# Kernel tuning notes

Hardware: AMD Instinct MI355X
Metric: run time of the kernel (lower is better)

Reference implementation:

```python
import jax, jax.numpy as jnp
import numpy as np

E, T, D_IN, D_INT = 8, 512, 7168, 2048


def setup_inputs() -> dict:
    key = jax.random.key(0)
    ks = jax.random.split(key, 7)
    return {
        "x": jax.random.normal(ks[0], (E, T, D_IN), dtype=jnp.float32),
        "w1": jax.random.normal(ks[1], (E, D_INT, D_IN), dtype=jnp.float32),
        "b1": jax.random.normal(ks[2], (E, D_INT), dtype=jnp.float32),
        "w3": jax.random.normal(ks[3], (E, D_INT, D_IN), dtype=jnp.float32),
        "b3": jax.random.normal(ks[4], (E, D_INT), dtype=jnp.float32),
        "w2": jax.random.normal(ks[5], (E, D_IN, D_INT), dtype=jnp.float32),
        "b2": jax.random.normal(ks[6], (E, D_IN), dtype=jnp.float32),
    }


def reference(x, w1, b1, w3, b3, w2, b2):
    # Batched (per-expert) SwiGLU FFN: w2(silu(w1(x)) * w3(x)), all with bias.
    # e: expert, t: token, d: in_channels, f: inter_channels
    h1 = jnp.einsum("etd,efd->etf", x, w1) + b1[:, None, :]  # [E,T,F]
    h3 = jnp.einsum("etd,efd->etf", x, w3) + b3[:, None, :]  # [E,T,F]
    g = jax.nn.silu(h1) * h3                                  # [E,T,F]
    return jnp.einsum("etf,edf->etd", g, w2) + b2[:, None, :]  # [E,T,D]
```

## Files before the change

kernel.cpp:

```cpp
#include <hip/hip_runtime.h>
#include <hip/hip_bf16.h>

#define NE 8
#define NT 512
#define DIN 7168
#define DINT 2048
#define BK 64

typedef __bf16 bf16x8 __attribute__((ext_vector_type(8)));
typedef float f32x4 __attribute__((ext_vector_type(4)));
typedef unsigned short ushort8v __attribute__((ext_vector_type(8)));

#define MFMA __builtin_amdgcn_mfma_f32_16x16x32_bf16

__device__ __forceinline__ int swz(int row, int k) {
    return (row << 6) + (((k >> 3) ^ (row & 7)) << 3) + (k & 7);
}

__device__ __forceinline__ ushort4 cvt4(float4 v) {
    ushort4 h;
    h.x = __builtin_bit_cast(unsigned short, (__bf16)v.x);
    h.y = __builtin_bit_cast(unsigned short, (__bf16)v.y);
    h.z = __builtin_bit_cast(unsigned short, (__bf16)v.z);
    h.w = __builtin_bit_cast(unsigned short, (__bf16)v.w);
    return h;
}

__device__ __forceinline__ void barrier_lgkm() {
    asm volatile("s_waitcnt lgkmcnt(0)" ::: "memory");
    __builtin_amdgcn_s_barrier();
}

__global__ __launch_bounds__(512, 2) void ffn_gate_up(
    const float* __restrict__ x, const float* __restrict__ w1,
    const float* __restrict__ b1, const float* __restrict__ w3,
    const float* __restrict__ b3, unsigned short* __restrict__ g) {
    __shared__ unsigned short As[2][256 * BK];
    __shared__ unsigned short B1s[2][128 * BK];
    __shared__ unsigned short B3s[2][128 * BK];

    const int tid = threadIdx.x;
    const int lane = tid & 63;
    const int wave = tid >> 6;
    const int wm = wave >> 1, wn = wave & 1;
    const int e = blockIdx.z;
    const int bn = blockIdx.x * 128;
    const int bm = blockIdx.y * 256;

    const char* xb = (const char*)x + ((size_t)e * NT * DIN + (size_t)bm * DIN) * 4;
    const char* w1c = (const char*)w1 + ((size_t)e * DINT * DIN + (size_t)bn * DIN) * 4;
    const char* w3c = (const char*)w3 + ((size_t)e * DINT * DIN + (size_t)bn * DIN) * 4;

    const int srow = tid >> 4;
    const int scol = (tid & 15) * 4;
    const int swb = swz(srow, scol);

    int xo[8];
#pragma unroll
    for (int p = 0; p < 8; ++p) xo[p] = ((p * 32 + srow) * DIN + scol) * 4;

    f32x4 acc1[4][4], acc3[4][4];
#pragma unroll
    for (int m = 0; m < 4; ++m)
#pragma unroll
        for (int n = 0; n < 4; ++n) {
            acc1[m][n] = (f32x4)0.0f;
            acc3[m][n] = (f32x4)0.0f;
        }

    float4 ra[8], rb1[4], rb3[4];

#pragma unroll
    for (int p = 0; p < 8; ++p) ra[p] = *(const float4*)(xb + xo[p]);
#pragma unroll
    for (int p = 0; p < 4; ++p) {
        rb1[p] = *(const float4*)(w1c + xo[p]);
        rb3[p] = *(const float4*)(w3c + xo[p]);
    }
#pragma unroll
    for (int p = 0; p < 8; ++p) *(ushort4*)&As[0][p * 2048 + swb] = cvt4(ra[p]);
#pragma unroll
    for (int p = 0; p < 4; ++p) {
        *(ushort4*)&B1s[0][p * 2048 + swb] = cvt4(rb1[p]);
        *(ushort4*)&B3s[0][p * 2048 + swb] = cvt4(rb3[p]);
    }
#pragma unroll
    for (int p = 0; p < 8; ++p) ra[p] = *(const float4*)(xb + xo[p] + BK * 4);
#pragma unroll
    for (int p = 0; p < 4; ++p) {
        rb1[p] = *(const float4*)(w1c + xo[p] + BK * 4);
        rb3[p] = *(const float4*)(w3c + xo[p] + BK * 4);
    }
    barrier_lgkm();

    const int l15 = lane & 15;
    const int kf0 = (lane >> 4) << 3;

    int cur = 0;
    const int NIT = DIN / BK;
    for (int t = 0; t < NIT; ++t) {
        const int nxt = cur ^ 1;
        const int kldB = ((t + 2 < NIT) ? (t + 2) * BK : (NIT - 1) * BK) * 4;
        const bool stage = (t < NIT - 1);
        bf16x8 af[4], bb[4];

#pragma unroll
        for (int m = 0; m < 4; ++m)
            af[m] = *(const bf16x8*)&As[cur][swz(wm * 64 + m * 16 + l15, kf0)];
#pragma unroll
        for (int n = 0; n < 4; ++n)
            bb[n] = *(const bf16x8*)&B1s[cur][swz(wn * 64 + n * 16 + l15, kf0)];
        if (stage) {
#pragma unroll
            for (int p = 0; p < 4; ++p) *(ushort4*)&As[nxt][p * 2048 + swb] = cvt4(ra[p]);
#pragma unroll
            for (int p = 0; p < 4; ++p) ra[p] = *(const float4*)(xb + xo[p] + kldB);
        }
        __builtin_amdgcn_s_setprio(1);
#pragma unroll
        for (int n = 0; n < 4; ++n)
#pragma unroll
            for (int m = 0; m < 4; ++m)
                acc1[m][n] = MFMA(af[m], bb[n], acc1[m][n], 0, 0, 0);
        __builtin_amdgcn_s_setprio(0);
        __builtin_amdgcn_sched_barrier(0);

#pragma unroll
        for (int n = 0; n < 4; ++n)
            bb[n] = *(const bf16x8*)&B3s[cur][swz(wn * 64 + n * 16 + l15, kf0)];
        if (stage) {
#pragma unroll
            for (int p = 4; p < 8; ++p) *(ushort4*)&As[nxt][p * 2048 + swb] = cvt4(ra[p]);
#pragma unroll
            for (int p = 4; p < 8; ++p) ra[p] = *(const float4*)(xb + xo[p] + kldB);
        }
        __builtin_amdgcn_s_setprio(1);
#pragma unroll
        for (int n = 0; n < 4; ++n)
#pragma unroll
            for (int m = 0; m < 4; ++m)
                acc3[m][n] = MFMA(af[m], bb[n], acc3[m][n], 0, 0, 0);
        __builtin_amdgcn_s_setprio(0);
        __builtin_amdgcn_sched_barrier(0);

#pragma unroll
        for (int m = 0; m < 4; ++m)
            af[m] = *(const bf16x8*)&As[cur][swz(wm * 64 + m * 16 + l15, 32 + kf0)];
#pragma unroll
        for (int n = 0; n < 4; ++n)
            bb[n] = *(const bf16x8*)&B1s[cur][swz(wn * 64 + n * 16 + l15, 32 + kf0)];
        if (stage) {
#pragma unroll
            for (int p = 0; p < 4; ++p) *(ushort4*)&B1s[nxt][p * 2048 + swb] = cvt4(rb1[p]);
#pragma unroll
            for (int p = 0; p < 4; ++p) rb1[p] = *(const float4*)(w1c + xo[p] + kldB);
        }
        __builtin_amdgcn_s_setprio(1);
#pragma unroll
        for (int n = 0; n < 4; ++n)
#pragma unroll
            for (int m = 0; m < 4; ++m)
                acc1[m][n] = MFMA(af[m], bb[n], acc1[m][n], 0, 0, 0);
        __builtin_amdgcn_s_setprio(0);
        __builtin_amdgcn_sched_barrier(0);

#pragma unroll
        for (int n = 0; n < 4; ++n)
            bb[n] = *(const bf16x8*)&B3s[cur][swz(wn * 64 + n * 16 + l15, 32 + kf0)];
        if (stage) {
#pragma unroll
            for (int p = 0; p < 4; ++p) *(ushort4*)&B3s[nxt][p * 2048 + swb] = cvt4(rb3[p]);
#pragma unroll
            for (int p = 0; p < 4; ++p) rb3[p] = *(const float4*)(w3c + xo[p] + kldB);
        }
        __builtin_amdgcn_s_setprio(1);
#pragma unroll
        for (int n = 0; n < 4; ++n)
#pragma unroll
            for (int m = 0; m < 4; ++m)
                acc3[m][n] = MFMA(af[m], bb[n], acc3[m][n], 0, 0, 0);
        __builtin_amdgcn_s_setprio(0);

        barrier_lgkm();
        cur = nxt;
    }

    float bias1[4], bias3[4];
#pragma unroll
    for (int n = 0; n < 4; ++n) {
        const int f = bn + wn * 64 + n * 16 + l15;
        bias1[n] = b1[e * DINT + f];
        bias3[n] = b3[e * DINT + f];
    }
#pragma unroll
    for (int m = 0; m < 4; ++m)
#pragma unroll
        for (int n = 0; n < 4; ++n) {
            const int f = bn + wn * 64 + n * 16 + l15;
#pragma unroll
            for (int j = 0; j < 4; ++j) {
                const int t = bm + wm * 64 + m * 16 + ((lane >> 4) << 2) + j;
                const float h1 = acc1[m][n][j] + bias1[n];
                const float h3 = acc3[m][n][j] + bias3[n];
                const float sg = h1 / (1.0f + __expf(-h1));
                g[(size_t)e * NT * DINT + (size_t)t * DINT + f] =
                    __builtin_bit_cast(unsigned short, (__bf16)(sg * h3));
            }
        }
}

__global__ __launch_bounds__(512, 2) void ffn_down(
    const unsigned short* __restrict__ g, const float* __restrict__ w2,
    const float* __restrict__ b2, float* __restrict__ out) {
    __shared__ unsigned short As[2][256 * BK];
    __shared__ unsigned short Bs[2][128 * BK];

    const int tid = threadIdx.x;
    const int lane = tid & 63;
    const int wave = tid >> 6;
    const int wm = wave >> 1, wn = wave & 1;
    const int e = blockIdx.z;
    const int bn = blockIdx.x * 128;
    const int bm = blockIdx.y * 256;

    const char* gc = (const char*)g + ((size_t)e * NT * DINT + (size_t)bm * DINT) * 2;
    const char* w2c = (const char*)w2 + ((size_t)e * DIN * DINT + (size_t)bn * DINT) * 4;

    const int arow = tid >> 3;
    const int acol = (tid & 7) * 8;
    const int brow = tid >> 4;
    const int bcol = (tid & 15) * 4;
    const int swA = swz(arow, acol);
    const int swB = swz(brow, bcol);

    int go[4], wo[4];
#pragma unroll
    for (int p = 0; p < 4; ++p) {
        go[p] = ((p * 64 + arow) * DINT + acol) * 2;
        wo[p] = ((p * 32 + brow) * DINT + bcol) * 4;
    }

    f32x4 acc[4][4];
#pragma unroll
    for (int m = 0; m < 4; ++m)
#pragma unroll
        for (int n = 0; n < 4; ++n) acc[m][n] = (f32x4)0.0f;

    ushort8v ga[4];
    float4 rb[4];

#pragma unroll
    for (int p = 0; p < 4; ++p) ga[p] = *(const ushort8v*)(gc + go[p]);
#pragma unroll
    for (int p = 0; p < 4; ++p) rb[p] = *(const float4*)(w2c + wo[p]);
#pragma unroll
    for (int p = 0; p < 4; ++p) *(ushort8v*)&As[0][p * 4096 + swA] = ga[p];
#pragma unroll
    for (int p = 0; p < 4; ++p) *(ushort4*)&Bs[0][p * 2048 + swB] = cvt4(rb[p]);
#pragma unroll
    for (int p = 0; p < 4; ++p) ga[p] = *(const ushort8v*)(gc + go[p] + BK * 2);
#pragma unroll
    for (int p = 0; p < 4; ++p) rb[p] = *(const float4*)(w2c + wo[p] + BK * 4);
    barrier_lgkm();

    const int l15 = lane & 15;
    const int kf0 = (lane >> 4) << 3;

    int cur = 0;
    const int NIT = DINT / BK;
    for (int t = 0; t < NIT; ++t) {
        const int nxt = cur ^ 1;
        const int kld = (t + 2 < NIT) ? (t + 2) * BK : (NIT - 1) * BK;
        const bool stage = (t < NIT - 1);
        bf16x8 af[4], bf[4];

#pragma unroll
        for (int m = 0; m < 4; ++m)
            af[m] = *(const bf16x8*)&As[cur][swz(wm * 64 + m * 16 + l15, kf0)];
#pragma unroll
        for (int n = 0; n < 4; ++n)
            bf[n] = *(const bf16x8*)&Bs[cur][swz(wn * 64 + n * 16 + l15, kf0)];
        if (stage) {
#pragma unroll
            for (int p = 0; p < 4; ++p) *(ushort8v*)&As[nxt][p * 4096 + swA] = ga[p];
#pragma unroll
            for (int p = 0; p < 4; ++p) ga[p] = *(const ushort8v*)(gc + go[p] + kld * 2);
        }
        __builtin_amdgcn_s_setprio(1);
#pragma unroll
        for (int n = 0; n < 4; ++n)
#pragma unroll
            for (int m = 0; m < 4; ++m)
                acc[m][n] = MFMA(af[m], bf[n], acc[m][n], 0, 0, 0);
        __builtin_amdgcn_s_setprio(0);
        __builtin_amdgcn_sched_barrier(0);

#pragma unroll
        for (int m = 0; m < 4; ++m)
            af[m] = *(const bf16x8*)&As[cur][swz(wm * 64 + m * 16 + l15, 32 + kf0)];
#pragma unroll
        for (int n = 0; n < 4; ++n)
            bf[n] = *(const bf16x8*)&Bs[cur][swz(wn * 64 + n * 16 + l15, 32 + kf0)];
        if (stage) {
#pragma unroll
            for (int p = 0; p < 4; ++p) *(ushort4*)&Bs[nxt][p * 2048 + swB] = cvt4(rb[p]);
#pragma unroll
            for (int p = 0; p < 4; ++p) rb[p] = *(const float4*)(w2c + wo[p] + kld * 4);
        }
        __builtin_amdgcn_s_setprio(1);
#pragma unroll
        for (int n = 0; n < 4; ++n)
#pragma unroll
            for (int m = 0; m < 4; ++m)
                acc[m][n] = MFMA(af[m], bf[n], acc[m][n], 0, 0, 0);
        __builtin_amdgcn_s_setprio(0);

        barrier_lgkm();
        cur = nxt;
    }

    float bias[4];
#pragma unroll
    for (int n = 0; n < 4; ++n) {
        const int d = bn + wn * 64 + n * 16 + l15;
        bias[n] = b2[e * DIN + d];
    }
#pragma unroll
    for (int m = 0; m < 4; ++m)
#pragma unroll
        for (int n = 0; n < 4; ++n) {
            const int d = bn + wn * 64 + n * 16 + l15;
#pragma unroll
            for (int j = 0; j < 4; ++j) {
                const int t = bm + wm * 64 + m * 16 + ((lane >> 4) << 2) + j;
                out[(size_t)e * NT * DIN + (size_t)t * DIN + d] = acc[m][n][j] + bias[n];
            }
        }
}

extern "C" void kernel_launch(void* const* d_in, const int* in_sizes, int n_in,
                              void* d_out, int out_size, void* d_ws, size_t ws_size,
                              hipStream_t stream) {
    const float* x = (const float*)d_in[0];
    const float* w1 = (const float*)d_in[1];
    const float* b1 = (const float*)d_in[2];
    const float* w3 = (const float*)d_in[3];
    const float* b3 = (const float*)d_in[4];
    const float* w2 = (const float*)d_in[5];
    const float* b2 = (const float*)d_in[6];
    float* out = (float*)d_out;
    unsigned short* g = (unsigned short*)d_ws;

    dim3 gridA(DINT / 128, NT / 256, NE);
    dim3 gridB(DIN / 128, NT / 256, NE);
    ffn_gate_up<<<gridA, dim3(512), 0, stream>>>(x, w1, b1, w3, b3, g);
    ffn_down<<<gridB, dim3(512), 0, stream>>>(g, w2, b2, out);
}
```

Measured before the change: 502.0 us.

## Use 8-wide LDS stores and per-phase barriers for ping-pong wave scheduling

Staging now has each thread load two adjacent float4s, 32 contiguous bytes per row, and write them to LDS as one 16-byte bf16x8 store instead of two 8-byte stores. This halves the LDS store instruction count. The single end-of-iteration barrier is replaced by s_barrier calls around every MFMA phase, so waves alternate between memory and compute in lockstep, a ping-pong schedule. Global loads now run unconditionally, clamped to the last tile. The extra barriers add sync overhead per iteration and may stall waves if the phases are unbalanced.

Measured after the change: 523.9 us. 4.4% more time.

```diff
diff --git a/kernel.cpp b/kernel.cpp
--- a/kernel.cpp
+++ b/kernel.cpp
@@ -17,19 +17,20 @@
     return (row << 6) + (((k >> 3) ^ (row & 7)) << 3) + (k & 7);
 }
 
-__device__ __forceinline__ ushort4 cvt4(float4 v) {
-    ushort4 h;
-    h.x = __builtin_bit_cast(unsigned short, (__bf16)v.x);
-    h.y = __builtin_bit_cast(unsigned short, (__bf16)v.y);
-    h.z = __builtin_bit_cast(unsigned short, (__bf16)v.z);
-    h.w = __builtin_bit_cast(unsigned short, (__bf16)v.w);
+__device__ __forceinline__ unsigned short b16(float f) {
+    return __builtin_bit_cast(unsigned short, (__bf16)f);
+}
+__device__ __forceinline__ ushort8v cvt8(float4 a, float4 b) {
+    ushort8v h;
+    h[0] = b16(a.x); h[1] = b16(a.y); h[2] = b16(a.z); h[3] = b16(a.w);
+    h[4] = b16(b.x); h[5] = b16(b.y); h[6] = b16(b.z); h[7] = b16(b.w);
     return h;
 }
 
-__device__ __forceinline__ void barrier_lgkm() {
-    asm volatile("s_waitcnt lgkmcnt(0)" ::: "memory");
-    __builtin_amdgcn_s_barrier();
-}
+#define PHASE_BAR()                                        \
+    __builtin_amdgcn_s_barrier();                          \
+    asm volatile("s_waitcnt lgkmcnt(0)" ::: "memory");     \
+    __builtin_amdgcn_sched_barrier(0)
 
 __global__ __launch_bounds__(512, 2) void ffn_gate_up(
     const float* __restrict__ x, const float* __restrict__ w1,
@@ -51,13 +52,16 @@
     const char* w1c = (const char*)w1 + ((size_t)e * DINT * DIN + (size_t)bn * DIN) * 4;
     const char* w3c = (const char*)w3 + ((size_t)e * DINT * DIN + (size_t)bn * DIN) * 4;
 
-    const int srow = tid >> 4;
-    const int scol = (tid & 15) * 4;
-    const int swb = swz(srow, scol);
-
-    int xo[8];
-#pragma unroll
-    for (int p = 0; p < 8; ++p) xo[p] = ((p * 32 + srow) * DIN + scol) * 4;
+    const int srow = tid >> 3;
+    const int sc8 = (tid & 7) * 8;
+    const int scB = (tid & 7) * 32;
+    const int swb = swz(srow, sc8);
+
+    int xoA[4], xoB[2];
+#pragma unroll
+    for (int p = 0; p < 4; ++p) xoA[p] = (p * 64 + srow) * DIN * 4 + scB;
+#pragma unroll
+    for (int p = 0; p < 2; ++p) xoB[p] = (p * 64 + srow) * DIN * 4 + scB;
 
     f32x4 acc1[4][4], acc3[4][4];
 #pragma unroll
@@ -71,27 +75,39 @@
     float4 ra[8], rb1[4], rb3[4];
 
 #pragma unroll
-    for (int p = 0; p < 8; ++p) ra[p] = *(const float4*)(xb + xo[p]);
-#pragma unroll
     for (int p = 0; p < 4; ++p) {
-        rb1[p] = *(const float4*)(w1c + xo[p]);
-        rb3[p] = *(const float4*)(w3c + xo[p]);
-    }
-#pragma unroll
-    for (int p = 0; p < 8; ++p) *(ushort4*)&As[0][p * 2048 + swb] = cvt4(ra[p]);
+        ra[2 * p] = *(const float4*)(xb + xoA[p]);
+        ra[2 * p + 1] = *(const float4*)(xb + xoA[p] + 16);
+    }
+#pragma unroll
+    for (int p = 0; p < 2; ++p) {
+        rb1[2 * p] = *(const float4*)(w1c + xoB[p]);
+        rb1[2 * p + 1] = *(const float4*)(w1c + xoB[p] + 16);
+        rb3[2 * p] = *(const float4*)(w3c + xoB[p]);
+        rb3[2 * p + 1] = *(const float4*)(w3c + xoB[p] + 16);
+    }
+#pragma unroll
+    for (int p = 0; p < 4; ++p)
+        *(ushort8v*)&As[0][p * 4096 + swb] = cvt8(ra[2 * p], ra[2 * p + 1]);
+#pragma unroll
+    for (int p = 0; p < 2; ++p) {
+        *(ushort8v*)&B1s[0][p * 4096 + swb] = cvt8(rb1[2 * p], rb1[2 * p + 1]);
+        *(ushort8v*)&B3s[0][p * 4096 + swb] = cvt8(rb3[2 * p], rb3[2 * p + 1]);
+    }
 #pragma unroll
     for (int p = 0; p < 4; ++p) {
-        *(ushort4*)&B1s[0][p * 2048 + swb] = cvt4(rb1[p]);
-        *(ushort4*)&B3s[0][p * 2048 + swb] = cvt4(rb3[p]);
-    }
-#pragma unroll
-    for (int p = 0; p < 8; ++p) ra[p] = *(const float4*)(xb + xo[p] + BK * 4);
-#pragma unroll
-    for (int p = 0; p < 4; ++p) {
-        rb1[p] = *(const float4*)(w1c + xo[p] + BK * 4);
-        rb3[p] = *(const float4*)(w3c + xo[p] + BK * 4);
-    }
-    barrier_lgkm();
+        ra[2 * p] = *(const float4*)(xb + xoA[p] + BK * 4);
+        ra[2 * p + 1] = *(const float4*)(xb + xoA[p] + BK * 4 + 16);
+    }
+#pragma unroll
+    for (int p = 0; p < 2; ++p) {
+        rb1[2 * p] = *(const float4*)(w1c + xoB[p] + BK * 4);
+        rb1[2 * p + 1] = *(const float4*)(w1c + xoB[p] + BK * 4 + 16);
+        rb3[2 * p] = *(const float4*)(w3c + xoB[p] + BK * 4);
+        rb3[2 * p + 1] = *(const float4*)(w3c + xoB[p] + BK * 4 + 16);
+    }
+    asm volatile("s_waitcnt lgkmcnt(0)" ::: "memory");
+    __builtin_amdgcn_s_barrier();
 
     const int l15 = lane & 15;
     const int kf0 = (lane >> 4) << 3;
@@ -100,7 +116,7 @@
     const int NIT = DIN / BK;
     for (int t = 0; t < NIT; ++t) {
         const int nxt = cur ^ 1;
-        const int kldB = ((t + 2 < NIT) ? (t + 2) * BK : (NIT - 1) * BK) * 4;
+        const int kldB = ((t + 2 < NIT) ? (t + 2) : (NIT - 1)) * BK * 4;
         const bool stage = (t < NIT - 1);
         bf16x8 af[4], bb[4];
 
@@ -111,11 +127,14 @@
         for (int n = 0; n < 4; ++n)
             bb[n] = *(const bf16x8*)&B1s[cur][swz(wn * 64 + n * 16 + l15, kf0)];
         if (stage) {
-#pragma unroll
-            for (int p = 0; p < 4; ++p) *(ushort4*)&As[nxt][p * 2048 + swb] = cvt4(ra[p]);
-#pragma unroll
-            for (int p = 0; p < 4; ++p) ra[p] = *(const float4*)(xb + xo[p] + kldB);
-        }
+            *(ushort8v*)&As[nxt][0 * 4096 + swb] = cvt8(ra[0], ra[1]);
+            *(ushort8v*)&As[nxt][1 * 4096 + swb] = cvt8(ra[2], ra[3]);
+        }
+        ra[0] = *(const float4*)(xb + xoA[0] + kldB);
+        ra[1] = *(const float4*)(xb + xoA[0] + kldB + 16);
+        ra[2] = *(const float4*)(xb + xoA[1] + kldB);
+        ra[3] = *(const float4*)(xb + xoA[1] + kldB + 16);
+        PHASE_BAR();
         __builtin_amdgcn_s_setprio(1);
 #pragma unroll
         for (int n = 0; n < 4; ++n)
@@ -123,17 +142,20 @@
             for (int m = 0; m < 4; ++m)
                 acc1[m][n] = MFMA(af[m], bb[n], acc1[m][n], 0, 0, 0);
         __builtin_amdgcn_s_setprio(0);
-        __builtin_amdgcn_sched_barrier(0);
+        __builtin_amdgcn_s_barrier();
 
 #pragma unroll
         for (int n = 0; n < 4; ++n)
             bb[n] = *(const bf16x8*)&B3s[cur][swz(wn * 64 + n * 16 + l15, kf0)];
         if (stage) {
-#pragma unroll
-            for (int p = 4; p < 8; ++p) *(ushort4*)&As[nxt][p * 2048 + swb] = cvt4(ra[p]);
-#pragma unroll
-            for (int p = 4; p < 8; ++p) ra[p] = *(const float4*)(xb + xo[p] + kldB);
-        }
+            *(ushort8v*)&As[nxt][2 * 4096 + swb] = cvt8(ra[4], ra[5]);
+            *(ushort8v*)&As[nxt][3 * 4096 + swb] = cvt8(ra[6], ra[7]);
+        }
+        ra[4] = *(const float4*)(xb + xoA[2] + kldB);
+        ra[5] = *(const float4*)(xb + xoA[2] + kldB + 16);
+        ra[6] = *(const float4*)(xb + xoA[3] + kldB);
+        ra[7] = *(const float4*)(xb + xoA[3] + kldB + 16);
+        PHASE_BAR();
         __builtin_amdgcn_s_setprio(1);
 #pragma unroll
         for (int n = 0; n < 4; ++n)
@@ -141,7 +163,7 @@
             for (int m = 0; m < 4; ++m)
                 acc3[m][n] = MFMA(af[m], bb[n], acc3[m][n], 0, 0, 0);
         __builtin_amdgcn_s_setprio(0);
-        __builtin_amdgcn_sched_barrier(0);
+        __builtin_amdgcn_s_barrier();
 
 #pragma unroll
         for (int m = 0; m < 4; ++m)
@@ -150,11 +172,14 @@
         for (int n = 0; n < 4; ++n)
             bb[n] = *(const bf16x8*)&B1s[cur][swz(wn * 64 + n * 16 + l15, 32 + kf0)];
         if (stage) {
-#pragma unroll
-            for (int p = 0; p < 4; ++p) *(ushort4*)&B1s[nxt][p * 2048 + swb] = cvt4(rb1[p]);
-#pragma unroll
-            for (int p = 0; p < 4; ++p) rb1[p] = *(const float4*)(w1c + xo[p] + kldB);
-        }
+            *(ushort8v*)&B1s[nxt][0 * 4096 + swb] = cvt8(rb1[0], rb1[1]);
+            *(ushort8v*)&B1s[nxt][1 * 4096 + swb] = cvt8(rb1[2], rb1[3]);
+        }
+        rb1[0] = *(const float4*)(w1c + xoB[0] + kldB);
+        rb1[1] = *(const float4*)(w1c + xoB[0] + kldB + 16);
+        rb1[2] = *(const float4*)(w1c + xoB[1] + kldB);
+        rb1[3] = *(const float4*)(w1c + xoB[1] + kldB + 16);
+        PHASE_BAR();
         __builtin_amdgcn_s_setprio(1);
 #pragma unroll
         for (int n = 0; n < 4; ++n)
@@ -162,17 +187,20 @@
             for (int m = 0; m < 4; ++m)
                 acc1[m][n] = MFMA(af[m], bb[n], acc1[m][n], 0, 0, 0);
         __builtin_amdgcn_s_setprio(0);
-        __builtin_amdgcn_sched_barrier(0);
+        __builtin_amdgcn_s_barrier();
 
 #pragma unroll
         for (int n = 0; n < 4; ++n)
             bb[n] = *(const bf16x8*)&B3s[cur][swz(wn * 64 + n * 16 + l15, 32 + kf0)];
         if (stage) {
-#pragma unroll
-            for (int p = 0; p < 4; ++p) *(ushort4*)&B3s[nxt][p * 2048 + swb] = cvt4(rb3[p]);
-#pragma unroll
-            for (int p = 0; p < 4; ++p) rb3[p] = *(const float4*)(w3c + xo[p] + kldB);
-        }
+            *(ushort8v*)&B3s[nxt][0 * 4096 + swb] = cvt8(rb3[0], rb3[1]);
+            *(ushort8v*)&B3s[nxt][1 * 4096 + swb] = cvt8(rb3[2], rb3[3]);
+        }
+        rb3[0] = *(const float4*)(w3c + xoB[0] + kldB);
+        rb3[1] = *(const float4*)(w3c + xoB[0] + kldB + 16);
+        rb3[2] = *(const float4*)(w3c + xoB[1] + kldB);
+        rb3[3] = *(const float4*)(w3c + xoB[1] + kldB + 16);
+        PHASE_BAR();
         __builtin_amdgcn_s_setprio(1);
 #pragma unroll
         for (int n = 0; n < 4; ++n)
@@ -180,8 +208,8 @@
             for (int m = 0; m < 4; ++m)
                 acc3[m][n] = MFMA(af[m], bb[n], acc3[m][n], 0, 0, 0);
         __builtin_amdgcn_s_setprio(0);
-
-        barrier_lgkm();
+        __builtin_amdgcn_s_barrier();
+
         cur = nxt;
     }
 
@@ -226,19 +254,15 @@
     const char* gc = (const char*)g + ((size_t)e * NT * DINT + (size_t)bm * DINT) * 2;
     const char* w2c = (const char*)w2 + ((size_t)e * DIN * DINT + (size_t)bn * DINT) * 4;
 
-    const int arow = tid >> 3;
-    const int acol = (tid & 7) * 8;
-    const int brow = tid >> 4;
-    const int bcol = (tid & 15) * 4;
-    const int swA = swz(arow, acol);
-    const int swB = swz(brow, bcol);
-
-    int go[4], wo[4];
-#pragma unroll
-    for (int p = 0; p < 4; ++p) {
-        go[p] = ((p * 64 + arow) * DINT + acol) * 2;
-        wo[p] = ((p * 32 + brow) * DINT + bcol) * 4;
-    }
+    const int srow = tid >> 3;
+    const int sc8 = (tid & 7) * 8;
+    const int sw8 = swz(srow, sc8);
+
+    int go[4], wo[2];
+#pragma unroll
+    for (int p = 0; p < 4; ++p) go[p] = (p * 64 + srow) * DINT * 2 + sc8 * 2;
+#pragma unroll
+    for (int p = 0; p < 2; ++p) wo[p] = (p * 64 + srow) * DINT * 4 + sc8 * 4;
 
     f32x4 acc[4][4];
 #pragma unroll
@@ -252,16 +276,24 @@
 #pragma unroll
     for (int p = 0; p < 4; ++p) ga[p] = *(const ushort8v*)(gc + go[p]);
 #pragma unroll
-    for (int p = 0; p < 4; ++p) rb[p] = *(const float4*)(w2c + wo[p]);
-#pragma unroll
-    for (int p = 0; p < 4; ++p) *(ushort8v*)&As[0][p * 4096 + swA] = ga[p];
-#pragma unroll
-    for (int p = 0; p < 4; ++p) *(ushort4*)&Bs[0][p * 2048 + swB] = cvt4(rb[p]);
+    for (int p = 0; p < 2; ++p) {
+        rb[2 * p] = *(const float4*)(w2c + wo[p]);
+        rb[2 * p + 1] = *(const float4*)(w2c + wo[p] + 16);
+    }
+#pragma unroll
+    for (int p = 0; p < 4; ++p) *(ushort8v*)&As[0][p * 4096 + sw8] = ga[p];
+#pragma unroll
+    for (int p = 0; p < 2; ++p)
+        *(ushort8v*)&Bs[0][p * 4096 + sw8] = cvt8(rb[2 * p], rb[2 * p + 1]);
 #pragma unroll
     for (int p = 0; p < 4; ++p) ga[p] = *(const ushort8v*)(gc + go[p] + BK * 2);
 #pragma unroll
-    for (int p = 0; p < 4; ++p) rb[p] = *(const float4*)(w2c + wo[p] + BK * 4);
-    barrier_lgkm();
+    for (int p = 0; p < 2; ++p) {
+        rb[2 * p] = *(const float4*)(w2c + wo[p] + BK * 4);
+        rb[2 * p + 1] = *(const float4*)(w2c + wo[p] + BK * 4 + 16);
+    }
+    asm volatile("s_waitcnt lgkmcnt(0)" ::: "memory");
+    __builtin_amdgcn_s_barrier();
 
     const int l15 = lane & 15;
     const int kf0 = (lane >> 4) << 3;
@@ -270,7 +302,7 @@
     const int NIT = DINT / BK;
     for (int t = 0; t < NIT; ++t) {
         const int nxt = cur ^ 1;
-        const int kld = (t + 2 < NIT) ? (t + 2) * BK : (NIT - 1) * BK;
+        const int kld = ((t + 2 < NIT) ? (t + 2) : (NIT - 1)) * BK;
         const bool stage = (t < NIT - 1);
         bf16x8 af[4], bf[4];
 
@@ -281,11 +313,15 @@
         for (int n = 0; n < 4; ++n)
             bf[n] = *(const bf16x8*)&Bs[cur][swz(wn * 64 + n * 16 + l15, kf0)];
         if (stage) {
-#pragma unroll
-            for (int p = 0; p < 4; ++p) *(ushort8v*)&As[nxt][p * 4096 + swA] = ga[p];
-#pragma unroll
-            for (int p = 0; p < 4; ++p) ga[p] = *(const ushort8v*)(gc + go[p] + kld * 2);
-        }
+            *(ushort8v*)&As[nxt][0 * 4096 + sw8] = ga[0];
+            *(ushort8v*)&As[nxt][1 * 4096 + sw8] = ga[1];
+            *(ushort8v*)&Bs[nxt][0 * 4096 + sw8] = cvt8(rb[0], rb[1]);
+        }
+        ga[0] = *(const ushort8v*)(gc + go[0] + kld * 2);
+        ga[1] = *(const ushort8v*)(gc + go[1] + kld * 2);
+        rb[0] = *(const float4*)(w2c + wo[0] + kld * 4);
+        rb[1] = *(const float4*)(w2c + wo[0] + kld * 4 + 16);
+        PHASE_BAR();
         __builtin_amdgcn_s_setprio(1);
 #pragma unroll
         for (int n = 0; n < 4; ++n)
@@ -293,7 +329,7 @@
             for (int m = 0; m < 4; ++m)
                 acc[m][n] = MFMA(af[m], bf[n], acc[m][n], 0, 0, 0);
         __builtin_amdgcn_s_setprio(0);
-        __builtin_amdgcn_sched_barrier(0);
+        __builtin_amdgcn_s_barrier();
 
 #pragma unroll
         for (int m = 0; m < 4; ++m)
@@ -302,11 +338,15 @@
         for (int n = 0; n < 4; ++n)
             bf[n] = *(const bf16x8*)&Bs[cur][swz(wn * 64 + n * 16 + l15, 32 + kf0)];
         if (stage) {
-#pragma unroll
-            for (int p = 0; p < 4; ++p) *(ushort4*)&Bs[nxt][p * 2048 + swB] = cvt4(rb[p]);
-#pragma unroll
-            for (int p = 0; p < 4; ++p) rb[p] = *(const float4*)(w2c + wo[p] + kld * 4);
-        }
+            *(ushort8v*)&As[nxt][2 * 4096 + sw8] = ga[2];
+            *(ushort8v*)&As[nxt][3 * 4096 + sw8] = ga[3];
+            *(ushort8v*)&Bs[nxt][1 * 4096 + sw8] = cvt8(rb[2], rb[3]);
+        }
+        ga[2] = *(const ushort8v*)(gc + go[2] + kld * 2);
+        ga[3] = *(const ushort8v*)(gc + go[3] + kld * 2);
+        rb[2] = *(const float4*)(w2c + wo[1] + kld * 4);
+        rb[3] = *(const float4*)(w2c + wo[1] + kld * 4 + 16);
+        PHASE_BAR();
         __builtin_amdgcn_s_setprio(1);
 #pragma unroll
         for (int n = 0; n < 4; ++n)
@@ -314,8 +354,8 @@
             for (int m = 0; m < 4; ++m)
                 acc[m][n] = MFMA(af[m], bf[n], acc[m][n], 0, 0, 0);
         __builtin_amdgcn_s_setprio(0);
-
-        barrier_lgkm();
+        __builtin_amdgcn_s_barrier();
+
         cur = nxt;
     }
 
```

## Warp-specialize gate/up kernel with dedicated producer waves for global-to-LDS staging

Applied to the files above, without the earlier changes.

Splits the gate/up GEMM block into 8 MFMA consumer waves and 4 producer waves. The producers load fp32 x/w1/w3 tiles, convert them to bf16 and write double-buffered LDS. The consumers only read LDS and issue MFMAs, meant to take load and convert latency off the compute waves. The block grows to 768 threads with a launch bound of 3 blocks per CU, which caps registers hard. Producers hold 32 float4 registers and consumers hold 128 accumulator floats, so spills are likely. LDS use of about 128KB per block already limits the CU to one block.

Result: slower. 568.3 us (+13.2%).

```diff
diff --git a/kernel.cpp b/kernel.cpp
--- a/kernel.cpp
+++ b/kernel.cpp
@@ -17,12 +17,18 @@
     return (row << 6) + (((k >> 3) ^ (row & 7)) << 3) + (k & 7);
 }
 
+__device__ __forceinline__ unsigned short b16(float f) {
+    return __builtin_bit_cast(unsigned short, (__bf16)f);
+}
+__device__ __forceinline__ ushort8v cvt8(float4 a, float4 b) {
+    ushort8v h;
+    h[0] = b16(a.x); h[1] = b16(a.y); h[2] = b16(a.z); h[3] = b16(a.w);
+    h[4] = b16(b.x); h[5] = b16(b.y); h[6] = b16(b.z); h[7] = b16(b.w);
+    return h;
+}
 __device__ __forceinline__ ushort4 cvt4(float4 v) {
     ushort4 h;
-    h.x = __builtin_bit_cast(unsigned short, (__bf16)v.x);
-    h.y = __builtin_bit_cast(unsigned short, (__bf16)v.y);
-    h.z = __builtin_bit_cast(unsigned short, (__bf16)v.z);
-    h.w = __builtin_bit_cast(unsigned short, (__bf16)v.w);
+    h.x = b16(v.x); h.y = b16(v.y); h.z = b16(v.z); h.w = b16(v.w);
     return h;
 }
 
@@ -31,7 +37,7 @@
     __builtin_amdgcn_s_barrier();
 }
 
-__global__ __launch_bounds__(512, 2) void ffn_gate_up(
+__global__ __launch_bounds__(768, 3) void ffn_gate_up(
     const float* __restrict__ x, const float* __restrict__ w1,
     const float* __restrict__ b1, const float* __restrict__ w3,
     const float* __restrict__ b3, unsigned short* __restrict__ g) {
@@ -42,171 +48,125 @@
     const int tid = threadIdx.x;
     const int lane = tid & 63;
     const int wave = tid >> 6;
-    const int wm = wave >> 1, wn = wave & 1;
     const int e = blockIdx.z;
     const int bn = blockIdx.x * 128;
     const int bm = blockIdx.y * 256;
-
-    const char* xb = (const char*)x + ((size_t)e * NT * DIN + (size_t)bm * DIN) * 4;
-    const char* w1c = (const char*)w1 + ((size_t)e * DINT * DIN + (size_t)bn * DIN) * 4;
-    const char* w3c = (const char*)w3 + ((size_t)e * DINT * DIN + (size_t)bn * DIN) * 4;
-
-    const int srow = tid >> 4;
-    const int scol = (tid & 15) * 4;
-    const int swb = swz(srow, scol);
-
-    int xo[8];
-#pragma unroll
-    for (int p = 0; p < 8; ++p) xo[p] = ((p * 32 + srow) * DIN + scol) * 4;
-
-    f32x4 acc1[4][4], acc3[4][4];
-#pragma unroll
-    for (int m = 0; m < 4; ++m)
-#pragma unroll
-        for (int n = 0; n < 4; ++n) {
-            acc1[m][n] = (f32x4)0.0f;
-            acc3[m][n] = (f32x4)0.0f;
-        }
-
-    float4 ra[8], rb1[4], rb3[4];
-
-#pragma unroll
-    for (int p = 0; p < 8; ++p) ra[p] = *(const float4*)(xb + xo[p]);
-#pragma unroll
-    for (int p = 0; p < 4; ++p) {
-        rb1[p] = *(const float4*)(w1c + xo[p]);
-        rb3[p] = *(const float4*)(w3c + xo[p]);
-    }
-#pragma unroll
-    for (int p = 0; p < 8; ++p) *(ushort4*)&As[0][p * 2048 + swb] = cvt4(ra[p]);
-#pragma unroll
-    for (int p = 0; p < 4; ++p) {
-        *(ushort4*)&B1s[0][p * 2048 + swb] = cvt4(rb1[p]);
-        *(ushort4*)&B3s[0][p * 2048 + swb] = cvt4(rb3[p]);
-    }
-#pragma unroll
-    for (int p = 0; p < 8; ++p) ra[p] = *(const float4*)(xb + xo[p] + BK * 4);
-#pragma unroll
-    for (int p = 0; p < 4; ++p) {
-        rb1[p] = *(const float4*)(w1c + xo[p] + BK * 4);
-        rb3[p] = *(const float4*)(w3c + xo[p] + BK * 4);
-    }
-    barrier_lgkm();
-
-    const int l15 = lane & 15;
-    const int kf0 = (lane >> 4) << 3;
-
-    int cur = 0;
     const int NIT = DIN / BK;
-    for (int t = 0; t < NIT; ++t) {
-        const int nxt = cur ^ 1;
-        const int kldB = ((t + 2 < NIT) ? (t + 2) * BK : (NIT - 1) * BK) * 4;
-        const bool stage = (t < NIT - 1);
-        bf16x8 af[4], bb[4];
-
+
+    if (wave < 8) {
+        const int wm = wave >> 1, wn = wave & 1;
+        const int l15 = lane & 15;
+        const int kf0 = (lane >> 4) << 3;
+
+        f32x4 acc1[4][4], acc3[4][4];
 #pragma unroll
         for (int m = 0; m < 4; ++m)
-            af[m] = *(const bf16x8*)&As[cur][swz(wm * 64 + m * 16 + l15, kf0)];
-#pragma unroll
-        for (int n = 0; n < 4; ++n)
-            bb[n] = *(const bf16x8*)&B1s[cur][swz(wn * 64 + n * 16 + l15, kf0)];
-        if (stage) {
-#pragma unroll
-            for (int p = 0; p < 4; ++p) *(ushort4*)&As[nxt][p * 2048 + swb] = cvt4(ra[p]);
-#pragma unroll
-            for (int p = 0; p < 4; ++p) ra[p] = *(const float4*)(xb + xo[p] + kldB);
-        }
-        __builtin_amdgcn_s_setprio(1);
-#pragma unroll
-        for (int n = 0; n < 4; ++n)
-#pragma unroll
-            for (int m = 0; m < 4; ++m)
-                acc1[m][n] = MFMA(af[m], bb[n], acc1[m][n], 0, 0, 0);
-        __builtin_amdgcn_s_setprio(0);
-        __builtin_amdgcn_sched_barrier(0);
-
-#pragma unroll
-        for (int n = 0; n < 4; ++n)
-            bb[n] = *(const bf16x8*)&B3s[cur][swz(wn * 64 + n * 16 + l15, kf0)];
-        if (stage) {
-#pragma unroll
-            for (int p = 4; p < 8; ++p) *(ushort4*)&As[nxt][p * 2048 + swb] = cvt4(ra[p]);
-#pragma unroll
-            for (int p = 4; p < 8; ++p) ra[p] = *(const float4*)(xb + xo[p] + kldB);
-        }
-        __builtin_amdgcn_s_setprio(1);
-#pragma unroll
-        for (int n = 0; n < 4; ++n)
-#pragma unroll
-            for (int m = 0; m < 4; ++m)
-                acc3[m][n] = MFMA(af[m], bb[n], acc3[m][n], 0, 0, 0);
-        __builtin_amdgcn_s_setprio(0);
-        __builtin_amdgcn_sched_barrier(0);
-
-#pragma unroll
-        for (int m = 0; m < 4; ++m)
-            af[m] = *(const bf16x8*)&As[cur][swz(wm * 64 + m * 16 + l15, 32 + kf0)];
-#pragma unroll
-        for (int n = 0; n < 4; ++n)
-            bb[n] = *(const bf16x8*)&B1s[cur][swz(wn * 64 + n * 16 + l15, 32 + kf0)];
-        if (stage) {
-#pragma unroll
-            for (int p = 0; p < 4; ++p) *(ushort4*)&B1s[nxt][p * 2048 + swb] = cvt4(rb1[p]);
-#pragma unroll
-            for (int p = 0; p < 4; ++p) rb1[p] = *(const float4*)(w1c + xo[p] + kldB);
-        }
-        __builtin_amdgcn_s_setprio(1);
-#pragma unroll
-        for (int n = 0; n < 4; ++n)
-#pragma unroll
-            for (int m = 0; m < 4; ++m)
-                acc1[m][n] = MFMA(af[m], bb[n], acc1[m][n], 0, 0, 0);
-        __builtin_amdgcn_s_setprio(0);
-        __builtin_amdgcn_sched_barrier(0);
-
-#pragma unroll
-        for (int n = 0; n < 4; ++n)
-            bb[n] = *(const bf16x8*)&B3s[cur][swz(wn * 64 + n * 16 + l15, 32 + kf0)];
-        if (stage) {
-#pragma unroll
-            for (int p = 0; p < 4; ++p) *(ushort4*)&B3s[nxt][p * 2048 + swb] = cvt4(rb3[p]);
-#pragma unroll
-            for (int p = 0; p < 4; ++p) rb3[p] = *(const float4*)(w3c + xo[p] + kldB);
-        }
-        __builtin_amdgcn_s_setprio(1);
-#pragma unroll
-        for (int n = 0; n < 4; ++n)
-#pragma unroll
-            for (int m = 0; m < 4; ++m)
-                acc3[m][n] = MFMA(af[m], bb[n], acc3[m][n], 0, 0, 0);
-        __builtin_amdgcn_s_setprio(0);
-
-        barrier_lgkm();
-        cur = nxt;
-    }
-
-    float bias1[4], bias3[4];
-#pragma unroll
-    for (int n = 0; n < 4; ++n) {
-        const int f = bn + wn * 64 + n * 16 + l15;
-        bias1[n] = b1[e * DINT + f];
-        bias3[n] = b3[e * DINT + f];
-    }
-#pragma unroll
-    for (int m = 0; m < 4; ++m)
+#pragma unroll
+            for (int n = 0; n < 4; ++n) {
+                acc1[m][n] = (f32x4)0.0f;
+                acc3[m][n] = (f32x4)0.0f;
+            }
+
+        __builtin_amdgcn_s_barrier();
+
+        int cur = 0;
+        for (int t = 0; t < NIT; ++t) {
+#pragma unroll
+            for (int ks = 0; ks < 2; ++ks) {
+                const int kf = ks * 32 + kf0;
+                bf16x8 af[4];
+#pragma unroll
+                for (int m = 0; m < 4; ++m)
+                    af[m] = *(const bf16x8*)&As[cur][swz(wm * 64 + m * 16 + l15, kf)];
+#pragma unroll
+                for (int n = 0; n < 4; ++n) {
+                    const bf16x8 b1f = *(const bf16x8*)&B1s[cur][swz(wn * 64 + n * 16 + l15, kf)];
+                    const bf16x8 b3f = *(const bf16x8*)&B3s[cur][swz(wn * 64 + n * 16 + l15, kf)];
+                    __builtin_amdgcn_s_setprio(1);
+#pragma unroll
+                    for (int m = 0; m < 4; ++m)
+                        acc1[m][n] = MFMA(af[m], b1f, acc1[m][n], 0, 0, 0);
+#pragma unroll
+                    for (int m = 0; m < 4; ++m)
+                        acc3[m][n] = MFMA(af[m], b3f, acc3[m][n], 0, 0, 0);
+                    __builtin_amdgcn_s_setprio(0);
+                }
+            }
+            __builtin_amdgcn_s_barrier();
+            cur ^= 1;
+        }
+
+        float bias1[4], bias3[4];
 #pragma unroll
         for (int n = 0; n < 4; ++n) {
             const int f = bn + wn * 64 + n * 16 + l15;
-#pragma unroll
-            for (int j = 0; j < 4; ++j) {
-                const int t = bm + wm * 64 + m * 16 + ((lane >> 4) << 2) + j;
-                const float h1 = acc1[m][n][j] + bias1[n];
-                const float h3 = acc3[m][n][j] + bias3[n];
-                const float sg = h1 / (1.0f + __expf(-h1));
-                g[(size_t)e * NT * DINT + (size_t)t * DINT + f] =
-                    __builtin_bit_cast(unsigned short, (__bf16)(sg * h3));
-            }
-        }
+            bias1[n] = b1[e * DINT + f];
+            bias3[n] = b3[e * DINT + f];
+        }
+#pragma unroll
+        for (int m = 0; m < 4; ++m)
+#pragma unroll
+            for (int n = 0; n < 4; ++n) {
+                const int f = bn + wn * 64 + n * 16 + l15;
+#pragma unroll
+                for (int j = 0; j < 4; ++j) {
+                    const int t = bm + wm * 64 + m * 16 + ((lane >> 4) << 2) + j;
+                    const float h1 = acc1[m][n][j] + bias1[n];
+                    const float h3 = acc3[m][n][j] + bias3[n];
+                    const float sg = h1 / (1.0f + __expf(-h1));
+                    g[(size_t)e * NT * DINT + (size_t)t * DINT + f] =
+                        __builtin_bit_cast(unsigned short, (__bf16)(sg * h3));
+                }
+            }
+    } else {
+        const int pw = wave - 8;
+        const char* xb = (const char*)x + ((size_t)e * NT * DIN + (size_t)bm * DIN) * 4;
+        const char* w1c = (const char*)w1 + ((size_t)e * DINT * DIN + (size_t)bn * DIN) * 4;
+        const char* w3c = (const char*)w3 + ((size_t)e * DINT * DIN + (size_t)bn * DIN) * 4;
+
+        const int lrow = lane >> 3;
+        const int gcol = (lane & 7) * 8;
+        const int rb = (pw == 1) ? 128 : 0;
+
+        const char* base = (pw < 2) ? xb : (pw == 2 ? w1c : w3c);
+        unsigned short* L0;
+        unsigned short* L1;
+        if (pw < 2) { L0 = &As[0][rb * 64]; L1 = &As[1][rb * 64]; }
+        else if (pw == 2) { L0 = B1s[0]; L1 = B1s[1]; }
+        else { L0 = B3s[0]; L1 = B3s[1]; }
+
+        const char* row0 = base + ((size_t)(rb + lrow) * DIN + gcol) * 4;
+        const int lidx0 = swz(lrow, gcol);
+
+        float4 fa[32];
+
+#pragma unroll
+        for (int p = 0; p < 16; ++p) {
+            fa[2 * p] = *(const float4*)(row0 + p * (8 * DIN * 4));
+            fa[2 * p + 1] = *(const float4*)(row0 + p * (8 * DIN * 4) + 16);
+        }
+#pragma unroll
+        for (int p = 0; p < 16; ++p)
+            *(ushort8v*)&L0[lidx0 + p * 512] = cvt8(fa[2 * p], fa[2 * p + 1]);
+#pragma unroll
+        for (int p = 0; p < 16; ++p) {
+            fa[2 * p] = *(const float4*)(row0 + p * (8 * DIN * 4) + BK * 4);
+            fa[2 * p + 1] = *(const float4*)(row0 + p * (8 * DIN * 4) + BK * 4 + 16);
+        }
+        barrier_lgkm();
+
+        for (int t = 0; t < NIT; ++t) {
+            unsigned short* lb = ((t + 1) & 1) ? L1 : L0;
+            const int kld = ((t + 2 < NIT) ? (t + 2) : (NIT - 1)) * BK * 4;
+#pragma unroll
+            for (int p = 0; p < 16; ++p) {
+                *(ushort8v*)&lb[lidx0 + p * 512] = cvt8(fa[2 * p], fa[2 * p + 1]);
+                fa[2 * p] = *(const float4*)(row0 + p * (8 * DIN * 4) + kld);
+                fa[2 * p + 1] = *(const float4*)(row0 + p * (8 * DIN * 4) + kld + 16);
+            }
+            barrier_lgkm();
+        }
+    }
 }
 
 __global__ __launch_bounds__(512, 2) void ffn_down(
@@ -353,6 +313,6 @@
 
     dim3 gridA(DINT / 128, NT / 256, NE);
     dim3 gridB(DIN / 128, NT / 256, NE);
-    ffn_gate_up<<<gridA, dim3(512), 0, stream>>>(x, w1, b1, w3, b3, g);
+    ffn_gate_up<<<gridA, dim3(768), 0, stream>>>(x, w1, b1, w3, b3, g);
     ffn_down<<<gridB, dim3(512), 0, stream>>>(g, w2, b2, out);
 }
```
